# Optimization experiments

Measured on AMD Instinct MI355X. Metric: run time of the kernel, lower is better.

The kernel has to match this reference:

```python
import jax, jax.numpy as jnp
import numpy as np

EPS = 1e-12  # matches torch.nn.functional.normalize default eps


def _l2norm(x, axis=-1):
    # F.normalize: x / max(||x||, eps)
    n = jnp.sqrt(jnp.sum(x * x, axis=axis, keepdims=True))
    return x / jnp.maximum(n, EPS)


def setup_inputs() -> dict:
    key = jax.random.key(0)
    k1, k2, k3 = jax.random.split(key, 3)
    batch, n_mels, time_steps = 32, 80, 4000
    num_codebooks, codebook_size, d = 2, 1024, 64
    mel = jax.random.normal(k1, (batch, n_mels, time_steps), dtype=jnp.float32)
    proj = jax.random.normal(k2, (num_codebooks, n_mels, d), dtype=jnp.float32)
    codebooks = jax.random.normal(k3, (num_codebooks, codebook_size, d), dtype=jnp.float32)
    return {"mel": mel, "proj": proj, "codebooks": codebooks}


def reference(mel, proj, codebooks):
    # mel: [b, n, t] -> [b, t, n]
    mel_t = jnp.transpose(mel, (0, 2, 1))
    # project for all codebooks at once: [c, b, t, d]
    p = jnp.einsum('btn,cnd->cbtd', mel_t, proj)
    p = _l2norm(p, axis=-1)
    cb = _l2norm(codebooks, axis=-1)  # [c, k, d]
    # cosine similarity: [c, b, t, k]
    sim = jnp.einsum('cbtd,ckd->cbtk', p, cb)
    codes = jnp.argmax(sim, axis=-1)  # [c, b, t]
    return codes
```

## Files before the change

kernel.cpp:

```cpp
#include <hip/hip_runtime.h>
#include <hip/hip_bf16.h>
#include <math.h>
#include <stdint.h>


#define B      32
#define NMELS  80
#define TSTEPS 4000
#define NCB    2
#define KCB    1024
#define DDIM   64
#define TPB    256
#define TM     64
#define KT     64
#define NKT    (KCB / KT)
#define PPAD   66

typedef short bf16x8 __attribute__((ext_vector_type(8)));
typedef float f32x4  __attribute__((ext_vector_type(4)));

#define WS_CB_OFF   8192
#define WS_NEEDED   (8192 + NCB*KCB*DDIM*2)

static __device__ __forceinline__ uint32_t bits(float f) {
    return __builtin_bit_cast(uint32_t, f);
}
static __device__ __forceinline__ float fbits(uint32_t u) {
    return __builtin_bit_cast(float, u);
}
static __device__ __forceinline__ uint32_t rne16(uint32_t u) {
    return (u + 0x7FFFu + ((u >> 16) & 1u)) >> 16;
}

__global__ __launch_bounds__(TPB) void rpq_prep(const float* __restrict__ cb,
                                                float* __restrict__ ws)
{
    const int idx = blockIdx.x * TPB + threadIdx.x;
    if (idx >= NCB * KCB) return;

    const float4* row = (const float4*)(cb + (size_t)idx * DDIM);
    float4 v[16];
    float ss = 0.f;
    #pragma unroll
    for (int i = 0; i < 16; ++i) {
        v[i] = row[i];
        ss += v[i].x*v[i].x + v[i].y*v[i].y + v[i].z*v[i].z + v[i].w*v[i].w;
    }
    const float inv = 1.0f / fmaxf(sqrtf(ss), 1e-12f);
    ws[idx] = inv;

    uint32_t dw[32];
    #pragma unroll
    for (int i = 0; i < 16; ++i) {
        dw[2*i]   = rne16(bits(v[i].x * inv)) | (rne16(bits(v[i].y * inv)) << 16);
        dw[2*i+1] = rne16(bits(v[i].z * inv)) | (rne16(bits(v[i].w * inv)) << 16);
    }
    uint4* dst = (uint4*)((char*)ws + WS_CB_OFF + (size_t)idx * 128);
    #pragma unroll
    for (int i = 0; i < 8; ++i)
        dst[i] = make_uint4(dw[4*i], dw[4*i+1], dw[4*i+2], dw[4*i+3]);
}

__global__ __launch_bounds__(TPB, 4) void rpq_main(
    const float* __restrict__ mel,
    const float* __restrict__ proj,
    const float* __restrict__ cb,
    const float* __restrict__ ws,
    int* __restrict__ out)
{
    const int tid  = threadIdx.x;
    const int b    = blockIdx.y;
    const int c    = blockIdx.z;
    const int t0   = blockIdx.x * TM;

    const int l    = tid & 63;
    const int wid  = tid >> 6;
    const int lrow = l & 15;
    const int lgrp = l >> 4;

    __shared__ union __align__(16) {
        float projS[NMELS * DDIM];
        struct {
            union {
                char cbuf[2][KT * 128];
                struct {
                    uint32_t cand[TM][17][2];
                    float    scv[TM][8];
                    int      sck[TM][8];
                } m;
            } a;
            float PL[TM * PPAD];
        } p2;
    } U;

    const char*  wscb   = (const char*)ws + WS_CB_OFF + (size_t)c * (KCB * 128);
    const float* invn_g = ws + (size_t)c * KCB;

    {
        const float4* src = (const float4*)(proj + (size_t)c * NMELS * DDIM);
        float4* dst = (float4*)U.projS;
        for (int i = tid; i < NMELS * DDIM / 4; i += TPB) dst[i] = src[i];
    }
    __syncthreads();

    const int srow = tid >> 2;
    const int sq   = tid & 3;
    uint4 ra0, ra1, rb0, rb1;
    {
        const uint4* gp0 = (const uint4*)(wscb + (size_t)srow * 128 + sq * 32);
        ra0 = gp0[0]; ra1 = gp0[1];
        const uint4* gp1 = (const uint4*)(wscb + (size_t)KT * 128
                                          + (size_t)srow * 128 + sq * 32);
        rb0 = gp1[0]; rb1 = gp1[1];
    }

    {
        const int tq = tid & 15;
        const int dg = tid >> 4;
        const int tbase  = t0 + tq * 4;
        const int tb_c   = (tbase <= TSTEPS - 4) ? tbase : (TSTEPS - 4);
        const float* mp  = mel + (size_t)b * NMELS * TSTEPS + tb_c;

        float Pa[4][4];
        #pragma unroll
        for (int i = 0; i < 4; ++i)
            #pragma unroll
            for (int j = 0; j < 4; ++j) Pa[i][j] = 0.f;

        for (int n = 0; n < NMELS; ++n) {
            const float4 m4 = *(const float4*)(mp + (size_t)n * TSTEPS);
            const float4 w  = *(const float4*)&U.projS[n * DDIM + dg * 4];
            Pa[0][0] = fmaf(m4.x, w.x, Pa[0][0]); Pa[0][1] = fmaf(m4.x, w.y, Pa[0][1]);
            Pa[0][2] = fmaf(m4.x, w.z, Pa[0][2]); Pa[0][3] = fmaf(m4.x, w.w, Pa[0][3]);
            Pa[1][0] = fmaf(m4.y, w.x, Pa[1][0]); Pa[1][1] = fmaf(m4.y, w.y, Pa[1][1]);
            Pa[1][2] = fmaf(m4.y, w.z, Pa[1][2]); Pa[1][3] = fmaf(m4.y, w.w, Pa[1][3]);
            Pa[2][0] = fmaf(m4.z, w.x, Pa[2][0]); Pa[2][1] = fmaf(m4.z, w.y, Pa[2][1]);
            Pa[2][2] = fmaf(m4.z, w.z, Pa[2][2]); Pa[2][3] = fmaf(m4.z, w.w, Pa[2][3]);
            Pa[3][0] = fmaf(m4.w, w.x, Pa[3][0]); Pa[3][1] = fmaf(m4.w, w.y, Pa[3][1]);
            Pa[3][2] = fmaf(m4.w, w.z, Pa[3][2]); Pa[3][3] = fmaf(m4.w, w.w, Pa[3][3]);
        }
        __syncthreads();

        #pragma unroll
        for (int i = 0; i < 4; ++i)
            *(float4*)&U.p2.PL[(tq * 4 + i) * PPAD + dg * 4] =
                make_float4(Pa[i][0], Pa[i][1], Pa[i][2], Pa[i][3]);
    }

    const int xw = (srow & 7) << 4;
    {
        char* base = &U.p2.a.cbuf[0][srow * 128];
        *(uint4*)(base + ((sq * 32)      ^ xw)) = ra0;
        *(uint4*)(base + ((sq * 32 + 16) ^ xw)) = ra1;
        const uint4* gp = (const uint4*)(wscb + (size_t)2 * (KT * 128)
                                         + (size_t)srow * 128 + sq * 32);
        ra0 = gp[0]; ra1 = gp[1];
    }
    __syncthreads();

    bf16x8 A0, A1;
    {
        const float* pr = &U.p2.PL[((wid << 4) + lrow) * PPAD];
        #pragma unroll
        for (int i = 0; i < 8; ++i) {
            A0[i] = (short)rne16(bits(pr[lgrp * 8 + i]));
            A1[i] = (short)rne16(bits(pr[32 + lgrp * 8 + i]));
        }
    }

    float m1[4], m2[4];
    #pragma unroll
    for (int r = 0; r < 4; ++r) { m1[r] = -INFINITY; m2[r] = -INFINITY; }
    uint32_t idxv = (uint32_t)(1023 - lrow);

    const int xr  = (lrow & 7) << 4;
    const int bo0 = (lgrp * 16) ^ xr;
    const int bo1 = (64 + lgrp * 16) ^ xr;

    #pragma unroll 2
    for (int kt = 0; kt < NKT; ++kt) {
        const char* buf = U.p2.a.cbuf[kt & 1];
        #pragma unroll
        for (int s = 0; s < 4; ++s) {
            const char* rowp = buf + (s * 16 + lrow) * 128;
            bf16x8 B0 = *(const bf16x8*)(rowp + bo0);
            bf16x8 B1 = *(const bf16x8*)(rowp + bo1);
            f32x4 acc = {0.f, 0.f, 0.f, 0.f};
            acc = __builtin_amdgcn_mfma_f32_16x16x32_bf16(A0, B0, acc, 0, 0, 0);
            acc = __builtin_amdgcn_mfma_f32_16x16x32_bf16(A1, B1, acc, 0, 0, 0);
            #pragma unroll
            for (int r = 0; r < 4; ++r) {
                const float pf = fbits((bits(acc[r]) & 0xFFFFFC00u)
                                     | (idxv & 0x3FFu));
                m2[r] = __builtin_amdgcn_fmed3f(pf, m1[r], m2[r]);
                m1[r] = fmaxf(pf, m1[r]);
            }
            idxv -= 16u;
        }
        if (kt + 1 < NKT) {
            char* base = &U.p2.a.cbuf[(kt + 1) & 1][srow * 128];
            if ((kt + 1) & 1) {
                *(uint4*)(base + ((sq * 32)      ^ xw)) = rb0;
                *(uint4*)(base + ((sq * 32 + 16) ^ xw)) = rb1;
                if (kt + 3 < NKT) {
                    const uint4* gp = (const uint4*)(wscb
                        + (size_t)(kt + 3) * (KT * 128)
                        + (size_t)srow * 128 + sq * 32);
                    rb0 = gp[0]; rb1 = gp[1];
                }
            } else {
                *(uint4*)(base + ((sq * 32)      ^ xw)) = ra0;
                *(uint4*)(base + ((sq * 32 + 16) ^ xw)) = ra1;
                if (kt + 3 < NKT) {
                    const uint4* gp = (const uint4*)(wscb
                        + (size_t)(kt + 3) * (KT * 128)
                        + (size_t)srow * 128 + sq * 32);
                    ra0 = gp[0]; ra1 = gp[1];
                }
            }
        }
        __syncthreads();
    }

    #pragma unroll
    for (int r = 0; r < 4; ++r) {
        const int trow = (wid << 4) + (lgrp << 2) + r;
        U.p2.a.m.cand[trow][lrow][0] = bits(m1[r]);
        U.p2.a.m.cand[trow][lrow][1] = bits(m2[r]);
    }
    __syncthreads();

    {
        const int t = tid & 63;
        const int j = wid;
        float c1 = -INFINITY, c2 = -INFINITY, c3 = -INFINITY, c4 = -INFINITY;
        float c5 = -INFINITY, c6 = -INFINITY, c7 = -INFINITY, c8 = -INFINITY;
        for (int i = 0; i < 16; ++i) {
            #pragma unroll
            for (int jj = 0; jj < 2; ++jj) {
                const float p = fbits(U.p2.a.m.cand[t][i][jj]);
                c8 = fmaxf(fminf(p, c7), c8);
                c7 = fmaxf(fminf(p, c6), c7);
                c6 = fmaxf(fminf(p, c5), c6);
                c5 = fmaxf(fminf(p, c4), c5);
                c4 = fmaxf(fminf(p, c3), c4);
                c3 = fmaxf(fminf(p, c2), c3);
                c2 = fmaxf(fminf(p, c1), c2);
                c1 = fmaxf(p, c1);
            }
        }
        const float sel0 = (j == 0) ? c1 : (j == 1) ? c3 : (j == 2) ? c5 : c7;
        const float sel1 = (j == 0) ? c2 : (j == 1) ? c4 : (j == 2) ? c6 : c8;
        const float* pr  = &U.p2.PL[t * PPAD];
        const float* cbc = cb + (size_t)c * KCB * DDIM;
        #pragma unroll
        for (int e = 0; e < 2; ++e) {
            const float sel = e ? sel1 : sel0;
            const int kj = 1023 - (int)(bits(sel) & 0x3FFu);
            const float* cbr = cbc + (size_t)kj * DDIM;
            float a0 = 0.f, a1 = 0.f, a2 = 0.f, a3 = 0.f;
            #pragma unroll
            for (int i = 0; i < 16; ++i) {
                float4 pv = *(const float4*)(pr + i * 4);
                float4 cv = *(const float4*)(cbr + i * 4);
                a0 = fmaf(pv.x, cv.x, a0); a1 = fmaf(pv.y, cv.y, a1);
                a2 = fmaf(pv.z, cv.z, a2); a3 = fmaf(pv.w, cv.w, a3);
            }
            U.p2.a.m.scv[t][2*j + e] = ((a0 + a1) + (a2 + a3)) * invn_g[kj];
            U.p2.a.m.sck[t][2*j + e] = kj;
        }
    }
    __syncthreads();

    if (tid < TM) {
        const int tg = t0 + tid;
        if (tg < TSTEPS) {
            float best = U.p2.a.m.scv[tid][0];
            int   bk   = U.p2.a.m.sck[tid][0];
            #pragma unroll
            for (int s2 = 1; s2 < 8; ++s2) {
                const float v = U.p2.a.m.scv[tid][s2];
                const int  kk = U.p2.a.m.sck[tid][s2];
                if (v > best || (v == best && kk < bk)) { best = v; bk = kk; }
            }
            out[((size_t)c * B + b) * TSTEPS + tg] = bk;
        }
    }
}

__global__ __launch_bounds__(TPB, 2) void rpq_fallback(
    const float* __restrict__ mel, const float* __restrict__ proj,
    const float* __restrict__ cb, int* __restrict__ out)
{
    const int tid = threadIdx.x;
    const int b = blockIdx.y, c = blockIdx.z;
    const int t0 = blockIdx.x * (TPB * 2) + tid;
    const int t1 = t0 + TPB;
    const int tc0 = (t0 < TSTEPS) ? t0 : (TSTEPS - 1);
    const int tc1 = (t1 < TSTEPS) ? t1 : (TSTEPS - 1);

    __shared__ union { float projS[NMELS*DDIM]; float cbS[2][64*DDIM]; } sh;
    __shared__ float invn[KCB];
    const float* cbc = cb + (size_t)c * KCB * DDIM;
    {
        const float4* src = (const float4*)(proj + (size_t)c * NMELS * DDIM);
        float4* dst = (float4*)sh.projS;
        for (int i = tid; i < NMELS*DDIM/4; i += TPB) dst[i] = src[i];
    }
    for (int j = 0; j < KCB/TPB; ++j) {
        const int k = j*TPB + tid;
        const float4* r = (const float4*)(cbc + (size_t)k * DDIM);
        float s = 0.f;
        #pragma unroll
        for (int i = 0; i < DDIM/4; ++i) {
            float4 v = r[i]; s += v.x*v.x + v.y*v.y + v.z*v.z + v.w*v.w;
        }
        invn[k] = 1.0f / fmaxf(sqrtf(s), 1e-12f);
    }
    float4 r0, r1, r2, r3;
    { const float4* g = (const float4*)cbc;
      r0 = g[tid]; r1 = g[tid+256]; r2 = g[tid+512]; r3 = g[tid+768]; }
    __syncthreads();
    float P0[DDIM], P1[DDIM];
    #pragma unroll
    for (int d = 0; d < DDIM; ++d) { P0[d] = 0.f; P1[d] = 0.f; }
    const float* mp = mel + (size_t)b * NMELS * TSTEPS;
    for (int n = 0; n < NMELS; ++n) {
        const float m0 = mp[(size_t)n*TSTEPS + tc0];
        const float m1_ = mp[(size_t)n*TSTEPS + tc1];
        const float4* ps = (const float4*)(sh.projS + n*DDIM);
        #pragma unroll
        for (int i = 0; i < DDIM/4; ++i) {
            float4 v = ps[i];
            P0[4*i+0]=fmaf(m0,v.x,P0[4*i+0]); P0[4*i+1]=fmaf(m0,v.y,P0[4*i+1]);
            P0[4*i+2]=fmaf(m0,v.z,P0[4*i+2]); P0[4*i+3]=fmaf(m0,v.w,P0[4*i+3]);
            P1[4*i+0]=fmaf(m1_,v.x,P1[4*i+0]); P1[4*i+1]=fmaf(m1_,v.y,P1[4*i+1]);
            P1[4*i+2]=fmaf(m1_,v.z,P1[4*i+2]); P1[4*i+3]=fmaf(m1_,v.w,P1[4*i+3]);
        }
    }
    __syncthreads();
    { float4* dst = (float4*)sh.cbS[0];
      dst[tid]=r0; dst[tid+256]=r1; dst[tid+512]=r2; dst[tid+768]=r3; }
    { const float4* g = (const float4*)(cbc + (size_t)64*DDIM);
      r0=g[tid]; r1=g[tid+256]; r2=g[tid+512]; r3=g[tid+768]; }
    __syncthreads();
    float best0 = -INFINITY, best1 = -INFINITY; int bi0 = 0, bi1 = 0;
    for (int kt = 0; kt < KCB/64; ++kt) {
        const int cur = kt & 1;
        const float* base = sh.cbS[cur];
        const int kbase = kt * 64;
        #pragma unroll 2
        for (int kk = 0; kk < 64; ++kk) {
            const float4* row = (const float4*)(base + kk*DDIM);
            float a0=0,a1=0,a2=0,a3=0,b0=0,b1=0,b2=0,b3=0;
            #pragma unroll
            for (int i = 0; i < DDIM/4; ++i) {
                float4 v = row[i];
                a0=fmaf(P0[4*i+0],v.x,a0); a1=fmaf(P0[4*i+1],v.y,a1);
                a2=fmaf(P0[4*i+2],v.z,a2); a3=fmaf(P0[4*i+3],v.w,a3);
                b0=fmaf(P1[4*i+0],v.x,b0); b1=fmaf(P1[4*i+1],v.y,b1);
                b2=fmaf(P1[4*i+2],v.z,b2); b3=fmaf(P1[4*i+3],v.w,b3);
            }
            const int k = kbase + kk;
            const float w = invn[k];
            const float s0 = ((a0+a1)+(a2+a3))*w;
            const float s1 = ((b0+b1)+(b2+b3))*w;
            if (s0 > best0) { best0 = s0; bi0 = k; }
            if (s1 > best1) { best1 = s1; bi1 = k; }
        }
        if (kt + 1 < KCB/64) {
            float4* dst = (float4*)sh.cbS[cur ^ 1];
            dst[tid]=r0; dst[tid+256]=r1; dst[tid+512]=r2; dst[tid+768]=r3;
            if (kt + 2 < KCB/64) {
                const float4* g = (const float4*)(cbc + (size_t)(kt+2)*64*DDIM);
                r0=g[tid]; r1=g[tid+256]; r2=g[tid+512]; r3=g[tid+768];
            }
        }
        __syncthreads();
    }
    const size_t ob = ((size_t)c * B + b) * TSTEPS;
    if (t0 < TSTEPS) out[ob + t0] = bi0;
    if (t1 < TSTEPS) out[ob + t1] = bi1;
}

extern "C" void kernel_launch(void* const* d_in, const int* in_sizes, int n_in,
                              void* d_out, int out_size, void* d_ws, size_t ws_size,
                              hipStream_t stream) {
    const float* mel  = (const float*)d_in[0];
    const float* proj = (const float*)d_in[1];
    const float* cb   = (const float*)d_in[2];
    int* out = (int*)d_out;

    if (ws_size >= (size_t)WS_NEEDED) {
        float* ws = (float*)d_ws;
        rpq_prep<<<dim3((NCB*KCB + TPB - 1)/TPB), dim3(TPB), 0, stream>>>(cb, ws);
        dim3 grid((TSTEPS + TM - 1) / TM, B, NCB);
        rpq_main<<<grid, dim3(TPB), 0, stream>>>(mel, proj, cb, ws, out);
    } else {
        dim3 grid((TSTEPS + TPB*2 - 1) / (TPB*2), B, NCB);
        rpq_fallback<<<grid, dim3(TPB), 0, stream>>>(mel, proj, cb, out);
    }
}
```

Measured before the change: 169.5 us.

## Double time tile per block to reuse codebook tiles across two MFMA row groups

Doubles the time rows per block from 64 to 128. Each wave now keeps two A fragments and issues four MFMAs for every codebook B fragment it loads, so codebook staging and the LDS reads are amortised over twice as many rows. The candidate buffer is transposed so the top-8 merge reads contiguously, and the rescoring step now splits candidates across two halves of threads. This costs more registers and LDS per block, occupancy drops (launch bounds 4 to 3), and the grid has half as many blocks.

Measured after the change: 171.0 us. No clear change (+0.9%).

```diff
diff --git a/kernel.cpp b/kernel.cpp
--- a/kernel.cpp
+++ b/kernel.cpp
@@ -11,7 +11,7 @@
 #define KCB    1024
 #define DDIM   64
 #define TPB    256
-#define TM     64
+#define TM     128
 #define KT     64
 #define NKT    (KCB / KT)
 #define PPAD   66
@@ -61,7 +61,7 @@
         dst[i] = make_uint4(dw[4*i], dw[4*i+1], dw[4*i+2], dw[4*i+3]);
 }
 
-__global__ __launch_bounds__(TPB, 4) void rpq_main(
+__global__ __launch_bounds__(TPB, 3) void rpq_main(
     const float* __restrict__ mel,
     const float* __restrict__ proj,
     const float* __restrict__ cb,
@@ -82,11 +82,11 @@
         float projS[NMELS * DDIM];
         struct {
             union {
-                char cbuf[2][KT * 128];
+                char     cbuf[2][KT * 128];
+                uint32_t candT[16][TM][2];
                 struct {
-                    uint32_t cand[TM][17][2];
-                    float    scv[TM][8];
-                    int      sck[TM][8];
+                    float scv[TM][9];
+                    int   sck[TM][9];
                 } m;
             } a;
             float PL[TM * PPAD];
@@ -117,33 +117,42 @@
     {
         const int tq = tid & 15;
         const int dg = tid >> 4;
-        const int tbase  = t0 + tq * 4;
-        const int tb_c   = (tbase <= TSTEPS - 4) ? tbase : (TSTEPS - 4);
+        const int tbase  = t0 + tq * 8;
+        const int tb_c   = (tbase <= TSTEPS - 8) ? tbase : (TSTEPS - 8);
         const float* mp  = mel + (size_t)b * NMELS * TSTEPS + tb_c;
 
-        float Pa[4][4];
-        #pragma unroll
-        for (int i = 0; i < 4; ++i)
+        float Pa[8][4];
+        #pragma unroll
+        for (int i = 0; i < 8; ++i)
             #pragma unroll
             for (int j = 0; j < 4; ++j) Pa[i][j] = 0.f;
 
         for (int n = 0; n < NMELS; ++n) {
-            const float4 m4 = *(const float4*)(mp + (size_t)n * TSTEPS);
+            const float4 mA = *(const float4*)(mp + (size_t)n * TSTEPS);
+            const float4 mB = *(const float4*)(mp + (size_t)n * TSTEPS + 4);
             const float4 w  = *(const float4*)&U.projS[n * DDIM + dg * 4];
-            Pa[0][0] = fmaf(m4.x, w.x, Pa[0][0]); Pa[0][1] = fmaf(m4.x, w.y, Pa[0][1]);
-            Pa[0][2] = fmaf(m4.x, w.z, Pa[0][2]); Pa[0][3] = fmaf(m4.x, w.w, Pa[0][3]);
-            Pa[1][0] = fmaf(m4.y, w.x, Pa[1][0]); Pa[1][1] = fmaf(m4.y, w.y, Pa[1][1]);
-            Pa[1][2] = fmaf(m4.y, w.z, Pa[1][2]); Pa[1][3] = fmaf(m4.y, w.w, Pa[1][3]);
-            Pa[2][0] = fmaf(m4.z, w.x, Pa[2][0]); Pa[2][1] = fmaf(m4.z, w.y, Pa[2][1]);
-            Pa[2][2] = fmaf(m4.z, w.z, Pa[2][2]); Pa[2][3] = fmaf(m4.z, w.w, Pa[2][3]);
-            Pa[3][0] = fmaf(m4.w, w.x, Pa[3][0]); Pa[3][1] = fmaf(m4.w, w.y, Pa[3][1]);
-            Pa[3][2] = fmaf(m4.w, w.z, Pa[3][2]); Pa[3][3] = fmaf(m4.w, w.w, Pa[3][3]);
+            Pa[0][0]=fmaf(mA.x,w.x,Pa[0][0]); Pa[0][1]=fmaf(mA.x,w.y,Pa[0][1]);
+            Pa[0][2]=fmaf(mA.x,w.z,Pa[0][2]); Pa[0][3]=fmaf(mA.x,w.w,Pa[0][3]);
+            Pa[1][0]=fmaf(mA.y,w.x,Pa[1][0]); Pa[1][1]=fmaf(mA.y,w.y,Pa[1][1]);
+            Pa[1][2]=fmaf(mA.y,w.z,Pa[1][2]); Pa[1][3]=fmaf(mA.y,w.w,Pa[1][3]);
+            Pa[2][0]=fmaf(mA.z,w.x,Pa[2][0]); Pa[2][1]=fmaf(mA.z,w.y,Pa[2][1]);
+            Pa[2][2]=fmaf(mA.z,w.z,Pa[2][2]); Pa[2][3]=fmaf(mA.z,w.w,Pa[2][3]);
+            Pa[3][0]=fmaf(mA.w,w.x,Pa[3][0]); Pa[3][1]=fmaf(mA.w,w.y,Pa[3][1]);
+            Pa[3][2]=fmaf(mA.w,w.z,Pa[3][2]); Pa[3][3]=fmaf(mA.w,w.w,Pa[3][3]);
+            Pa[4][0]=fmaf(mB.x,w.x,Pa[4][0]); Pa[4][1]=fmaf(mB.x,w.y,Pa[4][1]);
+            Pa[4][2]=fmaf(mB.x,w.z,Pa[4][2]); Pa[4][3]=fmaf(mB.x,w.w,Pa[4][3]);
+            Pa[5][0]=fmaf(mB.y,w.x,Pa[5][0]); Pa[5][1]=fmaf(mB.y,w.y,Pa[5][1]);
+            Pa[5][2]=fmaf(mB.y,w.z,Pa[5][2]); Pa[5][3]=fmaf(mB.y,w.w,Pa[5][3]);
+            Pa[6][0]=fmaf(mB.z,w.x,Pa[6][0]); Pa[6][1]=fmaf(mB.z,w.y,Pa[6][1]);
+            Pa[6][2]=fmaf(mB.z,w.z,Pa[6][2]); Pa[6][3]=fmaf(mB.z,w.w,Pa[6][3]);
+            Pa[7][0]=fmaf(mB.w,w.x,Pa[7][0]); Pa[7][1]=fmaf(mB.w,w.y,Pa[7][1]);
+            Pa[7][2]=fmaf(mB.w,w.z,Pa[7][2]); Pa[7][3]=fmaf(mB.w,w.w,Pa[7][3]);
         }
         __syncthreads();
 
         #pragma unroll
-        for (int i = 0; i < 4; ++i)
-            *(float4*)&U.p2.PL[(tq * 4 + i) * PPAD + dg * 4] =
+        for (int i = 0; i < 8; ++i)
+            *(float4*)&U.p2.PL[(tq * 8 + i) * PPAD + dg * 4] =
                 make_float4(Pa[i][0], Pa[i][1], Pa[i][2], Pa[i][3]);
     }
 
@@ -158,19 +167,22 @@
     }
     __syncthreads();
 
-    bf16x8 A0, A1;
-    {
-        const float* pr = &U.p2.PL[((wid << 4) + lrow) * PPAD];
+    bf16x8 A0[2], A1[2];
+    #pragma unroll
+    for (int p = 0; p < 2; ++p) {
+        const float* pr = &U.p2.PL[(p * 64 + (wid << 4) + lrow) * PPAD];
         #pragma unroll
         for (int i = 0; i < 8; ++i) {
-            A0[i] = (short)rne16(bits(pr[lgrp * 8 + i]));
-            A1[i] = (short)rne16(bits(pr[32 + lgrp * 8 + i]));
-        }
-    }
-
-    float m1[4], m2[4];
-    #pragma unroll
-    for (int r = 0; r < 4; ++r) { m1[r] = -INFINITY; m2[r] = -INFINITY; }
+            A0[p][i] = (short)rne16(bits(pr[lgrp * 8 + i]));
+            A1[p][i] = (short)rne16(bits(pr[32 + lgrp * 8 + i]));
+        }
+    }
+
+    float m1[2][4], m2[2][4];
+    #pragma unroll
+    for (int p = 0; p < 2; ++p)
+        #pragma unroll
+        for (int r = 0; r < 4; ++r) { m1[p][r] = -INFINITY; m2[p][r] = -INFINITY; }
     uint32_t idxv = (uint32_t)(1023 - lrow);
 
     const int xr  = (lrow & 7) << 4;
@@ -185,15 +197,22 @@
             const char* rowp = buf + (s * 16 + lrow) * 128;
             bf16x8 B0 = *(const bf16x8*)(rowp + bo0);
             bf16x8 B1 = *(const bf16x8*)(rowp + bo1);
-            f32x4 acc = {0.f, 0.f, 0.f, 0.f};
-            acc = __builtin_amdgcn_mfma_f32_16x16x32_bf16(A0, B0, acc, 0, 0, 0);
-            acc = __builtin_amdgcn_mfma_f32_16x16x32_bf16(A1, B1, acc, 0, 0, 0);
+            f32x4 accL = {0.f, 0.f, 0.f, 0.f};
+            f32x4 accH = {0.f, 0.f, 0.f, 0.f};
+            accL = __builtin_amdgcn_mfma_f32_16x16x32_bf16(A0[0], B0, accL, 0, 0, 0);
+            accH = __builtin_amdgcn_mfma_f32_16x16x32_bf16(A0[1], B0, accH, 0, 0, 0);
+            accL = __builtin_amdgcn_mfma_f32_16x16x32_bf16(A1[0], B1, accL, 0, 0, 0);
+            accH = __builtin_amdgcn_mfma_f32_16x16x32_bf16(A1[1], B1, accH, 0, 0, 0);
             #pragma unroll
             for (int r = 0; r < 4; ++r) {
-                const float pf = fbits((bits(acc[r]) & 0xFFFFFC00u)
-                                     | (idxv & 0x3FFu));
-                m2[r] = __builtin_amdgcn_fmed3f(pf, m1[r], m2[r]);
-                m1[r] = fmaxf(pf, m1[r]);
+                const float pfL = fbits((bits(accL[r]) & 0xFFFFFC00u)
+                                      | (idxv & 0x3FFu));
+                m2[0][r] = __builtin_amdgcn_fmed3f(pfL, m1[0][r], m2[0][r]);
+                m1[0][r] = fmaxf(pfL, m1[0][r]);
+                const float pfH = fbits((bits(accH[r]) & 0xFFFFFC00u)
+                                      | (idxv & 0x3FFu));
+                m2[1][r] = __builtin_amdgcn_fmed3f(pfH, m1[1][r], m2[1][r]);
+                m1[1][r] = fmaxf(pfH, m1[1][r]);
             }
             idxv -= 16u;
         }
@@ -223,22 +242,26 @@
     }
 
     #pragma unroll
-    for (int r = 0; r < 4; ++r) {
-        const int trow = (wid << 4) + (lgrp << 2) + r;
-        U.p2.a.m.cand[trow][lrow][0] = bits(m1[r]);
-        U.p2.a.m.cand[trow][lrow][1] = bits(m2[r]);
-    }
-    __syncthreads();
-
-    {
-        const int t = tid & 63;
-        const int j = wid;
+    for (int p = 0; p < 2; ++p)
+        #pragma unroll
+        for (int r = 0; r < 4; ++r) {
+            const int trow = p * 64 + (wid << 4) + (lgrp << 2) + r;
+            U.p2.a.candT[lrow][trow][0] = bits(m1[p][r]);
+            U.p2.a.candT[lrow][trow][1] = bits(m2[p][r]);
+        }
+    __syncthreads();
+
+    float se0, se1, se2, se3;
+    {
+        const int t  = tid & 127;
+        const int j2 = tid >> 7;
         float c1 = -INFINITY, c2 = -INFINITY, c3 = -INFINITY, c4 = -INFINITY;
         float c5 = -INFINITY, c6 = -INFINITY, c7 = -INFINITY, c8 = -INFINITY;
         for (int i = 0; i < 16; ++i) {
+            const uint2 pv2 = *(const uint2*)&U.p2.a.candT[i][t][0];
             #pragma unroll
             for (int jj = 0; jj < 2; ++jj) {
-                const float p = fbits(U.p2.a.m.cand[t][i][jj]);
+                const float p = fbits(jj ? pv2.y : pv2.x);
                 c8 = fmaxf(fminf(p, c7), c8);
                 c7 = fmaxf(fminf(p, c6), c7);
                 c6 = fmaxf(fminf(p, c5), c6);
@@ -249,14 +272,20 @@
                 c1 = fmaxf(p, c1);
             }
         }
-        const float sel0 = (j == 0) ? c1 : (j == 1) ? c3 : (j == 2) ? c5 : c7;
-        const float sel1 = (j == 0) ? c2 : (j == 1) ? c4 : (j == 2) ? c6 : c8;
+        se0 = j2 ? c5 : c1;  se1 = j2 ? c6 : c2;
+        se2 = j2 ? c7 : c3;  se3 = j2 ? c8 : c4;
+    }
+    __syncthreads();
+
+    {
+        const int t  = tid & 127;
+        const int j2 = tid >> 7;
         const float* pr  = &U.p2.PL[t * PPAD];
         const float* cbc = cb + (size_t)c * KCB * DDIM;
-        #pragma unroll
-        for (int e = 0; e < 2; ++e) {
-            const float sel = e ? sel1 : sel0;
-            const int kj = 1023 - (int)(bits(sel) & 0x3FFu);
+        const float sels[4] = { se0, se1, se2, se3 };
+        #pragma unroll
+        for (int e = 0; e < 4; ++e) {
+            const int kj = 1023 - (int)(bits(sels[e]) & 0x3FFu);
             const float* cbr = cbc + (size_t)kj * DDIM;
             float a0 = 0.f, a1 = 0.f, a2 = 0.f, a3 = 0.f;
             #pragma unroll
@@ -266,8 +295,8 @@
                 a0 = fmaf(pv.x, cv.x, a0); a1 = fmaf(pv.y, cv.y, a1);
                 a2 = fmaf(pv.z, cv.z, a2); a3 = fmaf(pv.w, cv.w, a3);
             }
-            U.p2.a.m.scv[t][2*j + e] = ((a0 + a1) + (a2 + a3)) * invn_g[kj];
-            U.p2.a.m.sck[t][2*j + e] = kj;
+            U.p2.a.m.scv[t][4*j2 + e] = ((a0 + a1) + (a2 + a3)) * invn_g[kj];
+            U.p2.a.m.sck[t][4*j2 + e] = kj;
         }
     }
     __syncthreads();
```
